# Kernel optimization log

Measured on AMD Instinct MI355X. Metric: run time of the kernel, lower is better.

The kernel has to match this reference:

```python
import jax, jax.numpy as jnp
import numpy as np

ENSEMBLE_MAX_MEAN = 0.5  # weight on max-pooled similarity
EPS = 1e-12


def _l2norm(x, axis):
    return x / jnp.sqrt(jnp.sum(x * x, axis=axis, keepdims=True) + EPS)


def setup_inputs() -> dict:
    key = jax.random.key(0)
    k1, k2 = jax.random.split(key)
    image_feat = jax.random.normal(k1, (8, 512, 32, 32), dtype=jnp.float32)  # [B,C,H,W]
    proto_emb = jax.random.normal(k2, (150, 32, 512), dtype=jnp.float32)    # [N,K,C]
    return {"image_feat": image_feat, "proto_emb": proto_emb}


def reference(image_feat, proto_emb):
    # cosine similarity branch of FreeDAMasker.forward_seg
    # image_feat: [B,C,H,W], proto_emb: [N,K,C]
    img = _l2norm(image_feat, axis=1)
    pro = _l2norm(proto_emb, axis=-1)
    # simmap: [B,N,K,H,W]
    simmap = jnp.einsum('bchw,nkc->bnkhw', img, pro)
    sim_max = jnp.max(simmap, axis=2)   # [B,N,H,W]
    sim_mean = jnp.mean(simmap, axis=2)  # [B,N,H,W]
    sim = ENSEMBLE_MAX_MEAN * sim_max + (1.0 - ENSEMBLE_MAX_MEAN) * sim_mean
    # sim2mask: deterministic=True, hard=False -> soft sigmoid mask
    soft_mask = jax.nn.sigmoid(sim)
    return soft_mask, sim
```

## Files before the change

### kernel.cpp

```cpp
#include <hip/hip_runtime.h>
#include <hip/hip_bf16.h>

#define NPROT 150
#define KPROT 32
#define CDIM  512
#define BDIM  8
#define HWDIM 1024
#define MDIM  (NPROT * KPROT)
#define PDIM  (BDIM * HWDIM)

typedef int i32x4 __attribute__((ext_vector_type(4)));

#define QSA 508.0f
#define QSB 24.0f
#define DEQAB (1.0f / (508.0f * 24.0f))

__device__ __forceinline__ int q8a(float x) {
  return __float2int_rn(fminf(fmaxf(x * QSA, -127.0f), 127.0f));
}
__device__ __forceinline__ int q8b(float x) {
  return __float2int_rn(fminf(fmaxf(x * QSB, -127.0f), 127.0f));
}
__device__ __forceinline__ unsigned int pack4(int a, int b, int c, int d) {
  return (unsigned int)((a & 255) | ((b & 255) << 8) | ((c & 255) << 16) | ((d & 255) << 24));
}

#define GLOAD_LDS16(gsrc, ldst) __builtin_amdgcn_global_load_lds(            \
    (const __attribute__((address_space(1))) void*)(gsrc),                   \
    (__attribute__((address_space(3))) void*)(ldst), 16, 0, 0)

__global__ __launch_bounds__(256) void prep_k(const float* __restrict__ img,
                                              const float* __restrict__ proto,
                                              char* __restrict__ Ai8,
                                              char* __restrict__ Bi8,
                                              float* __restrict__ invB) {
  __shared__ char tile[32][528];
  __shared__ float psum[8][32];
  int t   = threadIdx.x;
  int bid = blockIdx.x;
  if (bid >= 256) {
    int row  = (bid - 256) * 4 + (t >> 6);
    int lane = t & 63;
    const float4* rp = (const float4*)(proto + (size_t)row * CDIM);
    float4 v0 = rp[lane * 2];
    float4 v1 = rp[lane * 2 + 1];
    float ss = v0.x*v0.x + v0.y*v0.y + v0.z*v0.z + v0.w*v0.w
             + v1.x*v1.x + v1.y*v1.y + v1.z*v1.z + v1.w*v1.w;
    #pragma unroll
    for (int o = 32; o > 0; o >>= 1) ss += __shfl_xor(ss, o, 64);
    float inv = rsqrtf(ss + 1e-12f);
    uint2 o8;
    o8.x = pack4(q8a(v0.x*inv), q8a(v0.y*inv), q8a(v0.z*inv), q8a(v0.w*inv));
    o8.y = pack4(q8a(v1.x*inv), q8a(v1.y*inv), q8a(v1.z*inv), q8a(v1.w*inv));
    *(uint2*)(Ai8 + (size_t)row * CDIM + lane * 8) = o8;
    return;
  }
  int b   = bid >> 5;
  int hw0 = (bid & 31) << 5;
  int hwo = t & 31;
  int cg  = t >> 5;
  const float* base = img + ((size_t)b << 19) + hw0 + hwo;
  float ss = 0.f;
  #pragma unroll 4
  for (int i = 0; i < 64; i += 4) {
    int c = cg * 64 + i;
    float x0 = base[(size_t)(c + 0) << 10];
    float x1 = base[(size_t)(c + 1) << 10];
    float x2 = base[(size_t)(c + 2) << 10];
    float x3 = base[(size_t)(c + 3) << 10];
    ss += x0*x0 + x1*x1 + x2*x2 + x3*x3;
    *(unsigned int*)&tile[hwo][c] = pack4(q8b(x0), q8b(x1), q8b(x2), q8b(x3));
  }
  psum[cg][hwo] = ss;
  __syncthreads();
  if (t < 32) {
    float s = 0.f;
    #pragma unroll
    for (int j = 0; j < 8; ++j) s += psum[j][t];
    invB[((size_t)b << 10) + hw0 + t] = rsqrtf(s + 1e-12f);
  }
  #pragma unroll
  for (int it = 0; it < 4; ++it) {
    int gi  = it * 256 + t;
    int pix = gi >> 5, gr = gi & 31;
    int4 v = *(const int4*)&tile[pix][gr * 16];
    *(int4*)(Bi8 + (((size_t)b << 10) + hw0 + pix) * CDIM + gr * 16) = v;
  }
}

__global__ __launch_bounds__(256, 4) void gemm_k(const char* __restrict__ Ai8,
                                                 const char* __restrict__ Bi8,
                                                 const float* __restrict__ invB,
                                                 float* __restrict__ out) {
  __shared__ __align__(16) char smem[(64 + 256) * 128];
  char* As = smem;
  char* Bs = smem + 64 * 128;

  int t    = threadIdx.x;
  int lane = t & 63;
  int w    = t >> 6;
  int lr   = lane & 15;
  int lg   = lane >> 4;

  int bid = blockIdx.x;
  int xcd = bid & 7;
  int idx = bid >> 3;
  int bp  = (xcd << 2) + idx / 75;
  int bm  = idx % 75;
  int m0  = bm * 64;
  int p0  = bp * 256;

  i32x4 acc[4][4] = {};

  const char* Ab = Ai8 + (size_t)m0 * CDIM;
  const char* Bb = Bi8 + (size_t)p0 * CDIM;

  for (int c0 = 0; c0 < CDIM; c0 += 128) {
    #pragma unroll
    for (int it = 0; it < 2; ++it) {
      int gi  = it * 256 + t;
      int row = gi >> 3, g = gi & 7;
      int gs  = g ^ (row & 7);
      GLOAD_LDS16(Ab + (size_t)row * CDIM + c0 + gs * 16, As + gi * 16);
    }
    #pragma unroll
    for (int it = 0; it < 8; ++it) {
      int gi  = it * 256 + t;
      int row = gi >> 3, g = gi & 7;
      int gs  = g ^ (row & 7);
      GLOAD_LDS16(Bb + (size_t)row * CDIM + c0 + gs * 16, Bs + gi * 16);
    }
    __syncthreads();

    #pragma unroll
    for (int ks = 0; ks < 2; ++ks) {
      int gbase = ks * 4 + lg;
      i32x4 a4[4], b4[4];
      #pragma unroll
      for (int f = 0; f < 4; ++f) {
        int row = f * 16 + lr;
        a4[f] = *(const i32x4*)(As + row * 128 + (gbase ^ (row & 7)) * 16);
      }
      #pragma unroll
      for (int f = 0; f < 4; ++f) {
        int row = w * 64 + f * 16 + lr;
        b4[f] = *(const i32x4*)(Bs + row * 128 + (gbase ^ (row & 7)) * 16);
      }
      #pragma unroll
      for (int fm = 0; fm < 4; ++fm)
        #pragma unroll
        for (int fp = 0; fp < 4; ++fp)
          acc[fm][fp] = __builtin_amdgcn_mfma_i32_16x16x64_i8(a4[fm], b4[fp], acc[fm][fp], 0, 0, 0);
    }
    __syncthreads();
  }

  #pragma unroll
  for (int gi2 = 0; gi2 < 2; ++gi2) {
    #pragma unroll
    for (int fp = 0; fp < 4; ++fp) {
      float mx = -1e30f, sm = 0.f;
      #pragma unroll
      for (int fm = 2 * gi2; fm < 2 * gi2 + 2; ++fm)
        #pragma unroll
        for (int r = 0; r < 4; ++r) {
          float v = (float)acc[fm][fp][r];
          mx = fmaxf(mx, v);
          sm += v;
        }
      mx = fmaxf(mx, __shfl_xor(mx, 16, 64));
      mx = fmaxf(mx, __shfl_xor(mx, 32, 64));
      sm += __shfl_xor(sm, 16, 64);
      sm += __shfl_xor(sm, 32, 64);
      if (lg == 0) {
        int p  = p0 + w * 64 + fp * 16 + lr;
        float scale = DEQAB * invB[p];
        float sim   = (0.5f * mx + sm * (0.5f / 32.0f)) * scale;
        float mask  = 1.0f / (1.0f + __expf(-sim));
        int n  = bm * 2 + gi2;
        int b  = p >> 10, hw = p & 1023;
        size_t o = ((size_t)(b * NPROT + n) << 10) + hw;
        out[o] = mask;
        out[(size_t)(BDIM * NPROT * HWDIM) + o] = sim;
      }
    }
  }
}

extern "C" void kernel_launch(void* const* d_in, const int* in_sizes, int n_in,
                              void* d_out, int out_size, void* d_ws, size_t ws_size,
                              hipStream_t stream) {
  const float* img   = (const float*)d_in[0];
  const float* proto = (const float*)d_in[1];
  float* out = (float*)d_out;
  char*  Ai8  = (char*)d_ws;
  char*  Bi8  = Ai8 + (size_t)MDIM * CDIM;
  float* invB = (float*)(Bi8 + (size_t)PDIM * CDIM);

  prep_k<<<256 + MDIM / 4, 256, 0, stream>>>(img, proto, Ai8, Bi8, invB);
  gemm_k<<<2400, 256, 0, stream>>>(Ai8, Bi8, invB, out);
}
```

Measured before the change: 41.01 us.

## Pre-swizzle int8 operands into MFMA fragment layout and load directly to registers

The prep kernel now writes the quantized prototype and image matrices in a fragment-major layout, so each lane's 16-byte MFMA operand sits contiguously. The GEMM kernel drops the LDS staging, the global_load_lds path and the barriers, and reads A and B fragments straight from global memory into registers for all four K-steps. This removes LDS traffic and synchronisation. In exchange, every wave re-reads the shared A tile from global or L2 instead of sharing it through LDS, and register pressure rises, so the occupancy hint drops from 4 to 3.

```diff
diff --git a/kernel.cpp b/kernel.cpp
--- a/kernel.cpp
+++ b/kernel.cpp
@@ -15,6 +15,7 @@
 #define QSB 24.0f
 #define DEQAB (1.0f / (508.0f * 24.0f))
 
+
 __device__ __forceinline__ int q8a(float x) {
   return __float2int_rn(fminf(fmaxf(x * QSA, -127.0f), 127.0f));
 }
@@ -25,14 +26,10 @@
   return (unsigned int)((a & 255) | ((b & 255) << 8) | ((c & 255) << 16) | ((d & 255) << 24));
 }
 
-#define GLOAD_LDS16(gsrc, ldst) __builtin_amdgcn_global_load_lds(            \
-    (const __attribute__((address_space(1))) void*)(gsrc),                   \
-    (__attribute__((address_space(3))) void*)(ldst), 16, 0, 0)
-
 __global__ __launch_bounds__(256) void prep_k(const float* __restrict__ img,
                                               const float* __restrict__ proto,
-                                              char* __restrict__ Ai8,
-                                              char* __restrict__ Bi8,
+                                              char* __restrict__ Aq,
+                                              char* __restrict__ Bq,
                                               float* __restrict__ invB) {
   __shared__ char tile[32][528];
   __shared__ float psum[8][32];
@@ -52,7 +49,8 @@
     uint2 o8;
     o8.x = pack4(q8a(v0.x*inv), q8a(v0.y*inv), q8a(v0.z*inv), q8a(v0.w*inv));
     o8.y = pack4(q8a(v1.x*inv), q8a(v1.y*inv), q8a(v1.z*inv), q8a(v1.w*inv));
-    *(uint2*)(Ai8 + (size_t)row * CDIM + lane * 8) = o8;
+    size_t off = ((size_t)(row >> 4) * 32 + (lane >> 1)) * 256 + (row & 15) * 16 + (lane & 1) * 8;
+    *(uint2*)(Aq + off) = o8;
     return;
   }
   int b   = bid >> 5;
@@ -79,82 +77,59 @@
     for (int j = 0; j < 8; ++j) s += psum[j][t];
     invB[((size_t)b << 10) + hw0 + t] = rsqrtf(s + 1e-12f);
   }
+  int p16base = (((b << 10) + hw0) >> 4);
   #pragma unroll
   for (int it = 0; it < 4; ++it) {
-    int gi  = it * 256 + t;
-    int pix = gi >> 5, gr = gi & 31;
+    int pixlo = t & 15;
+    int gsel  = t >> 4;
+    int gr    = (it & 1) * 16 + gsel;
+    int pix   = (it >> 1) * 16 + pixlo;
     int4 v = *(const int4*)&tile[pix][gr * 16];
-    *(int4*)(Bi8 + (((size_t)b << 10) + hw0 + pix) * CDIM + gr * 16) = v;
+    *(int4*)(Bq + ((size_t)(p16base + (it >> 1)) * 32 + gr) * 256 + pixlo * 16) = v;
   }
 }
 
-__global__ __launch_bounds__(256, 4) void gemm_k(const char* __restrict__ Ai8,
-                                                 const char* __restrict__ Bi8,
+__global__ __launch_bounds__(256, 3) void gemm_k(const char* __restrict__ Aq,
+                                                 const char* __restrict__ Bq,
                                                  const float* __restrict__ invB,
                                                  float* __restrict__ out) {
-  __shared__ __align__(16) char smem[(64 + 256) * 128];
-  char* As = smem;
-  char* Bs = smem + 64 * 128;
-
   int t    = threadIdx.x;
   int lane = t & 63;
   int w    = t >> 6;
-  int lr   = lane & 15;
-  int lg   = lane >> 4;
 
   int bid = blockIdx.x;
   int xcd = bid & 7;
   int idx = bid >> 3;
   int bp  = (xcd << 2) + idx / 75;
   int bm  = idx % 75;
-  int m0  = bm * 64;
-  int p0  = bp * 256;
+
+  const char* Ab = Aq + (size_t)(bm * 4) * 8192;
+  const char* Bb = Bq + (size_t)(bp * 16 + w * 4) * 8192;
 
   i32x4 acc[4][4] = {};
 
-  const char* Ab = Ai8 + (size_t)m0 * CDIM;
-  const char* Bb = Bi8 + (size_t)p0 * CDIM;
-
-  for (int c0 = 0; c0 < CDIM; c0 += 128) {
+  #pragma unroll
+  for (int s = 0; s < 4; ++s) {
+    i32x4 a4[2][4], b4[2][4];
     #pragma unroll
-    for (int it = 0; it < 2; ++it) {
-      int gi  = it * 256 + t;
-      int row = gi >> 3, g = gi & 7;
-      int gs  = g ^ (row & 7);
-      GLOAD_LDS16(Ab + (size_t)row * CDIM + c0 + gs * 16, As + gi * 16);
-    }
-    #pragma unroll
-    for (int it = 0; it < 8; ++it) {
-      int gi  = it * 256 + t;
-      int row = gi >> 3, g = gi & 7;
-      int gs  = g ^ (row & 7);
-      GLOAD_LDS16(Bb + (size_t)row * CDIM + c0 + gs * 16, Bs + gi * 16);
-    }
-    __syncthreads();
-
-    #pragma unroll
-    for (int ks = 0; ks < 2; ++ks) {
-      int gbase = ks * 4 + lg;
-      i32x4 a4[4], b4[4];
+    for (int ks = 0; ks < 2; ++ks)
       #pragma unroll
       for (int f = 0; f < 4; ++f) {
-        int row = f * 16 + lr;
-        a4[f] = *(const i32x4*)(As + row * 128 + (gbase ^ (row & 7)) * 16);
+        a4[ks][f] = *(const i32x4*)(Ab + (size_t)f * 8192 + (s * 8 + ks * 4) * 256 + lane * 16);
+        b4[ks][f] = *(const i32x4*)(Bb + (size_t)f * 8192 + (s * 8 + ks * 4) * 256 + lane * 16);
       }
-      #pragma unroll
-      for (int f = 0; f < 4; ++f) {
-        int row = w * 64 + f * 16 + lr;
-        b4[f] = *(const i32x4*)(Bs + row * 128 + (gbase ^ (row & 7)) * 16);
-      }
+    #pragma unroll
+    for (int ks = 0; ks < 2; ++ks)
       #pragma unroll
       for (int fm = 0; fm < 4; ++fm)
         #pragma unroll
         for (int fp = 0; fp < 4; ++fp)
-          acc[fm][fp] = __builtin_amdgcn_mfma_i32_16x16x64_i8(a4[fm], b4[fp], acc[fm][fp], 0, 0, 0);
-    }
-    __syncthreads();
+          acc[fm][fp] = __builtin_amdgcn_mfma_i32_16x16x64_i8(a4[ks][fm], b4[ks][fp], acc[fm][fp], 0, 0, 0);
   }
 
+  int lr = lane & 15;
+  int lg = lane >> 4;
+  int p0 = bp * 256;
   #pragma unroll
   for (int gi2 = 0; gi2 < 2; ++gi2) {
     #pragma unroll
@@ -193,10 +168,10 @@
   const float* img   = (const float*)d_in[0];
   const float* proto = (const float*)d_in[1];
   float* out = (float*)d_out;
-  char*  Ai8  = (char*)d_ws;
-  char*  Bi8  = Ai8 + (size_t)MDIM * CDIM;
-  float* invB = (float*)(Bi8 + (size_t)PDIM * CDIM);
+  char*  Aq   = (char*)d_ws;
+  char*  Bq   = Aq + (size_t)300 * 8192;
+  float* invB = (float*)(Bq + (size_t)512 * 8192);
 
-  prep_k<<<256 + MDIM / 4, 256, 0, stream>>>(img, proto, Ai8, Bi8, invB);
-  gemm_k<<<2400, 256, 0, stream>>>(Ai8, Bi8, invB, out);
+  prep_k<<<256 + MDIM / 4, 256, 0, stream>>>(img, proto, Aq, Bq, invB);
+  gemm_k<<<2400, 256, 0, stream>>>(Aq, Bq, invB, out);
 }
```

Result: slower. 46.77 us (+14.0%).
